# Performance work log

Hardware: AMD Instinct MI355X
Metric: run time of the kernel (lower is better)

The kernel has to match this reference:

```python
import jax, jax.numpy as jnp
import numpy as np

B, W = 32, 8            # batch, context window (2*winsize)
NCH, NCO = 4, 8         # padded chars / compos per target word
N_WORD, N_CHAR, N_COMPO, DIM = 32000, 8000, 1000, 300
N_NEG = int(N_WORD ** 0.75)  # 2392, per original: int(n_word ** neg_sample)
PAD = 1                 # idx == 1 is masked out in build_embedding
EPS = 1e-32


def setup_inputs() -> dict:
    key = jax.random.key(0)
    ks = jax.random.split(key, 7)
    return {
        "word_emb": jax.random.normal(ks[0], (N_WORD, DIM), jnp.float32) * 0.01,
        "char_emb": jax.random.normal(ks[1], (N_CHAR, DIM), jnp.float32) * 0.01,
        "compo_emb": jax.random.normal(ks[2], (N_COMPO, DIM), jnp.float32) * 0.01,
        "chars": jax.random.randint(ks[3], (B, NCH), 0, N_CHAR),
        "compos": jax.random.randint(ks[4], (B, NCO), 0, N_COMPO),
        "ctx_words": jax.random.randint(ks[5], (B, W), 0, N_WORD),
        "noise": jax.random.randint(ks[6], (B, W, N_NEG), 0, N_WORD),
    }


def _bag(emb, idx):
    # masked embedding-bag: sum emb[idx] over last idx axis where idx != PAD
    vecs = emb[idx]  # [..., L, DIM]
    mask = (idx != PAD)[..., None].astype(emb.dtype)
    return (vecs * mask).sum(-2)


def reference(word_emb, char_emb, compo_emb, chars, compos, ctx_words, noise):
    # prediction vector = char-bag + compo-bag   -> [B, DIM]
    tgt = _bag(char_emb, chars) + _bag(compo_emb, compos)
    # context word vectors (single idx, masked)  -> [B, W, DIM]
    ctx = _bag(word_emb, ctx_words[:, :, None])
    # positive term: sum log sigmoid(tgt . ctx)
    s_pos = jnp.einsum("bd,bwd->bw", tgt, ctx)
    log_target = jnp.log(jax.nn.sigmoid(s_pos)).sum()
    # negative-sampling term over noise word embeddings [B, W, N_NEG, DIM]
    noise_vec = word_emb[noise]
    s_neg = jnp.einsum("bd,bwnd->bwn", tgt, noise_vec)
    sum_log_noise = jnp.log(jax.nn.sigmoid(-s_neg) + EPS).sum()
    loss = log_target + sum_log_noise
    return -loss / B
```

## Files before the change

### kernel.cpp

```cpp
#include <hip/hip_runtime.h>

#define N_WORD 32000
#define DIM    300
#define KP     320
#define LROW   328
#define BQ     32
#define WW     8
#define NNEG   2392
#define PERB   (WW*NNEG)
#define NTOT   (BQ*PERB)
#define VB     64
#define NGEMB  (N_WORD/VB)
#define NBLK3  1024

typedef __attribute__((ext_vector_type(8))) short short8;
typedef __attribute__((ext_vector_type(4))) float f32x4;

__device__ __forceinline__ unsigned f2b2(float lo, float hi) {
  unsigned ul = __builtin_bit_cast(unsigned, lo);
  unsigned uh = __builtin_bit_cast(unsigned, hi);
  ul = (ul + 0x7FFF + ((ul >> 16) & 1)) >> 16;
  uh = (uh + 0x7FFF + ((uh >> 16) & 1));
  return (ul & 0xFFFFu) | (uh & 0xFFFF0000u);
}
__device__ __forceinline__ unsigned short f2b(float f) {
  unsigned u = __builtin_bit_cast(unsigned, f);
  return (unsigned short)((u + 0x7FFF + ((u >> 16) & 1)) >> 16);
}

__global__ __launch_bounds__(256) void prep_kernel(
    const float* __restrict__ char_emb, const float* __restrict__ compo_emb,
    const int* __restrict__ chars, const int* __restrict__ compos,
    unsigned short* __restrict__ tgt_bf) {
  int b = blockIdx.x;
  for (int d = threadIdx.x; d < KP; d += 256) {
    float a = 0.f;
    if (d < DIM) {
      #pragma unroll
      for (int j = 0; j < 4; ++j) {
        int c = chars[b*4 + j];
        if (c != 1) a += char_emb[(size_t)c*DIM + d];
      }
      #pragma unroll
      for (int j = 0; j < 8; ++j) {
        int c = compos[b*8 + j];
        if (c != 1) a += compo_emb[(size_t)c*DIM + d];
      }
    }
    tgt_bf[b*KP + d] = (d < DIM) ? f2b(a) : (unsigned short)0;
  }
}

__global__ __launch_bounds__(256) void s_gemm_kernel(
    const float4* __restrict__ w4, const unsigned* __restrict__ tgtbf2,
    float* __restrict__ S) {
  __shared__ unsigned short wt[VB][LROW];
  __shared__ unsigned short tt[BQ][LROW];
  int tid = threadIdx.x, wv = tid >> 6, lane = tid & 63;
  int vbase = blockIdx.x * VB;

  for (int idx = tid; idx < VB*75; idx += 256) {
    float4 x = w4[(size_t)vbase*75 + idx];
    int row = idx / 75, col = idx - row*75;
    unsigned* dst = (unsigned*)&wt[row][col*4];
    dst[0] = f2b2(x.x, x.y);
    dst[1] = f2b2(x.z, x.w);
  }
  if (tid < VB) {
    unsigned* dst = (unsigned*)&wt[tid][300];
    #pragma unroll
    for (int j = 0; j < 10; ++j) dst[j] = 0;
  }
  for (int idx = tid; idx < BQ*(KP/2); idx += 256) {
    int row = idx / (KP/2), kk = idx - row*(KP/2);
    ((unsigned*)&tt[row][0])[kk] = tgtbf2[idx];
  }
  __syncthreads();

  int ln = lane & 15, g = lane >> 4;
  const unsigned short* brow  = &wt[wv*16 + ln][g*8];
  const unsigned short* arow0 = &tt[ln][g*8];
  const unsigned short* arow1 = &tt[16 + ln][g*8];
  f32x4 acc0 = {0.f,0.f,0.f,0.f}, acc1 = {0.f,0.f,0.f,0.f};
  #pragma unroll
  for (int kb = 0; kb < KP/32; ++kb) {
    short8 bf = *(const short8*)(brow  + kb*32);
    short8 a0 = *(const short8*)(arow0 + kb*32);
    short8 a1 = *(const short8*)(arow1 + kb*32);
    acc0 = __builtin_amdgcn_mfma_f32_16x16x32_bf16(a0, bf, acc0, 0, 0, 0);
    acc1 = __builtin_amdgcn_mfma_f32_16x16x32_bf16(a1, bf, acc1, 0, 0, 0);
  }

  int v = vbase + wv*16 + ln;
  #pragma unroll
  for (int r = 0; r < 4; ++r) {
    int b0 = g*4 + r;
    S[(size_t)b0*N_WORD + v]        = acc0[r];
    S[(size_t)(b0 + 16)*N_WORD + v] = acc1[r];
  }
}

__global__ __launch_bounds__(256) void loss_kernel(
    const float* __restrict__ S, const int* __restrict__ noise,
    const int* __restrict__ ctx, float* __restrict__ partials) {
  float a = 0.f;
  for (int i = blockIdx.x*256 + threadIdx.x; i < NTOT; i += 256*NBLK3) {
    int b = i / PERB;
    int idx = noise[i];
    float s = S[(size_t)b*N_WORD + idx];
    a += __logf(1.f/(1.f + __expf(s)) + 1e-32f);
  }
  if (blockIdx.x == 0) {
    int i = threadIdx.x;
    int c = ctx[i];
    float s = (c == 1) ? 0.f : S[(size_t)(i >> 3)*N_WORD + c];
    a += __logf(1.f/(1.f + __expf(-s)));
  }
  #pragma unroll
  for (int off = 32; off > 0; off >>= 1) a += __shfl_down(a, off);
  __shared__ float wsum[4];
  int lane = threadIdx.x & 63, wid = threadIdx.x >> 6;
  if (lane == 0) wsum[wid] = a;
  __syncthreads();
  if (threadIdx.x == 0)
    partials[blockIdx.x] = wsum[0] + wsum[1] + wsum[2] + wsum[3];
}

__global__ __launch_bounds__(256) void final_kernel(
    const float* __restrict__ partials, float* __restrict__ out) {
  double a = 0.0;
  for (int i = threadIdx.x; i < NBLK3; i += 256) a += (double)partials[i];
  #pragma unroll
  for (int off = 32; off > 0; off >>= 1) a += __shfl_down(a, off);
  __shared__ double w2[4];
  int lane = threadIdx.x & 63, wid = threadIdx.x >> 6;
  if (lane == 0) w2[wid] = a;
  __syncthreads();
  if (threadIdx.x == 0)
    out[0] = (float)(-(w2[0] + w2[1] + w2[2] + w2[3]) / (double)BQ);
}

extern "C" void kernel_launch(void* const* d_in, const int* in_sizes, int n_in,
                              void* d_out, int out_size, void* d_ws, size_t ws_size,
                              hipStream_t stream) {
  const float* word_emb  = (const float*)d_in[0];
  const float* char_emb  = (const float*)d_in[1];
  const float* compo_emb = (const float*)d_in[2];
  const int*   chars     = (const int*)d_in[3];
  const int*   compos    = (const int*)d_in[4];
  const int*   ctx       = (const int*)d_in[5];
  const int*   noise     = (const int*)d_in[6];
  float* out = (float*)d_out;

  char* ws = (char*)d_ws;
  unsigned short* tgt_bf   = (unsigned short*)(ws);
  float*          S        = (float*)(ws + 20480);
  float*          partials = (float*)(ws + 20480 + 4096000);

  prep_kernel<<<BQ, 256, 0, stream>>>(char_emb, compo_emb, chars, compos, tgt_bf);
  s_gemm_kernel<<<NGEMB, 256, 0, stream>>>(
      (const float4*)word_emb, (const unsigned*)tgt_bf, S);
  loss_kernel<<<NBLK3, 256, 0, stream>>>(S, noise, ctx, partials);
  final_kernel<<<1, 256, 0, stream>>>(partials, out);
}
```

Before: 32.99 us.

## Drop LDS staging in S GEMM and fuse final reduction via fixed-point atomics

The GEMM kernel now reads word embedding rows straight from global memory into MFMA operands and converts them to bf16 in registers, with no shared-memory staging or barrier. It also reads target vectors directly from global memory and raises occupancy through launch bounds. The separate final reduction kernel is removed: each loss block adds a fixed-point encoded partial with a 64-bit atomic, and the last block to finish writes the output. This saves one launch and the LDS round trip, at the cost of less coalesced global loads and some fixed-point quantization of the partial sums.

New measurement: 58.40 us. 77.0% more time.

```diff
diff --git a/kernel.cpp b/kernel.cpp
--- a/kernel.cpp
+++ b/kernel.cpp
@@ -3,15 +3,13 @@
 #define N_WORD 32000
 #define DIM    300
 #define KP     320
-#define LROW   328
 #define BQ     32
 #define WW     8
 #define NNEG   2392
 #define PERB   (WW*NNEG)
 #define NTOT   (BQ*PERB)
-#define VB     64
-#define NGEMB  (N_WORD/VB)
 #define NBLK3  1024
+#define FSCALE 268435456.0
 
 typedef __attribute__((ext_vector_type(8))) short short8;
 typedef __attribute__((ext_vector_type(4))) float f32x4;
@@ -31,7 +29,9 @@
 __global__ __launch_bounds__(256) void prep_kernel(
     const float* __restrict__ char_emb, const float* __restrict__ compo_emb,
     const int* __restrict__ chars, const int* __restrict__ compos,
-    unsigned short* __restrict__ tgt_bf) {
+    unsigned short* __restrict__ tgt_bf,
+    unsigned long long* __restrict__ acc, int* __restrict__ cnt) {
+  if (blockIdx.x == 0 && threadIdx.x == 0) { *acc = 0ULL; *cnt = 0; }
   int b = blockIdx.x;
   for (int d = threadIdx.x; d < KP; d += 256) {
     float a = 0.f;
@@ -51,47 +51,46 @@
   }
 }
 
-__global__ __launch_bounds__(256) void s_gemm_kernel(
-    const float4* __restrict__ w4, const unsigned* __restrict__ tgtbf2,
+__global__ __launch_bounds__(256, 2) void s_gemm_kernel(
+    const float* __restrict__ w, const unsigned short* __restrict__ tgt_bf,
     float* __restrict__ S) {
-  __shared__ unsigned short wt[VB][LROW];
-  __shared__ unsigned short tt[BQ][LROW];
   int tid = threadIdx.x, wv = tid >> 6, lane = tid & 63;
-  int vbase = blockIdx.x * VB;
+  int ln = lane & 15, g = lane >> 4;
+  int v = blockIdx.x*64 + wv*16 + ln;
+  const float* rp = w + (size_t)v*DIM;
+  const unsigned short* ar0 = tgt_bf + ln*KP;
+  const unsigned short* ar1 = tgt_bf + (16 + ln)*KP;
 
-  for (int idx = tid; idx < VB*75; idx += 256) {
-    float4 x = w4[(size_t)vbase*75 + idx];
-    int row = idx / 75, col = idx - row*75;
-    unsigned* dst = (unsigned*)&wt[row][col*4];
-    dst[0] = f2b2(x.x, x.y);
-    dst[1] = f2b2(x.z, x.w);
-  }
-  if (tid < VB) {
-    unsigned* dst = (unsigned*)&wt[tid][300];
-    #pragma unroll
-    for (int j = 0; j < 10; ++j) dst[j] = 0;
-  }
-  for (int idx = tid; idx < BQ*(KP/2); idx += 256) {
-    int row = idx / (KP/2), kk = idx - row*(KP/2);
-    ((unsigned*)&tt[row][0])[kk] = tgtbf2[idx];
-  }
-  __syncthreads();
-
-  int ln = lane & 15, g = lane >> 4;
-  const unsigned short* brow  = &wt[wv*16 + ln][g*8];
-  const unsigned short* arow0 = &tt[ln][g*8];
-  const unsigned short* arow1 = &tt[16 + ln][g*8];
   f32x4 acc0 = {0.f,0.f,0.f,0.f}, acc1 = {0.f,0.f,0.f,0.f};
   #pragma unroll
-  for (int kb = 0; kb < KP/32; ++kb) {
-    short8 bf = *(const short8*)(brow  + kb*32);
-    short8 a0 = *(const short8*)(arow0 + kb*32);
-    short8 a1 = *(const short8*)(arow1 + kb*32);
+  for (int kb = 0; kb < 9; ++kb) {
+    const float* p = rp + kb*32 + g*8;
+    float4 f0 = *(const float4*)p;
+    float4 f1 = *(const float4*)(p + 4);
+    short8 bf;
+    unsigned* bu = (unsigned*)&bf;
+    bu[0] = f2b2(f0.x, f0.y); bu[1] = f2b2(f0.z, f0.w);
+    bu[2] = f2b2(f1.x, f1.y); bu[3] = f2b2(f1.z, f1.w);
+    short8 a0 = *(const short8*)(ar0 + kb*32 + g*8);
+    short8 a1 = *(const short8*)(ar1 + kb*32 + g*8);
+    acc0 = __builtin_amdgcn_mfma_f32_16x16x32_bf16(a0, bf, acc0, 0, 0, 0);
+    acc1 = __builtin_amdgcn_mfma_f32_16x16x32_bf16(a1, bf, acc1, 0, 0, 0);
+  }
+  {
+    int k0 = 288 + g*8;
+    float4 f0 = {0.f,0.f,0.f,0.f}, f1 = {0.f,0.f,0.f,0.f};
+    if (k0 < 300)     f0 = *(const float4*)(rp + k0);
+    if (k0 + 4 < 300) f1 = *(const float4*)(rp + k0 + 4);
+    short8 bf;
+    unsigned* bu = (unsigned*)&bf;
+    bu[0] = f2b2(f0.x, f0.y); bu[1] = f2b2(f0.z, f0.w);
+    bu[2] = f2b2(f1.x, f1.y); bu[3] = f2b2(f1.z, f1.w);
+    short8 a0 = *(const short8*)(ar0 + 288 + g*8);
+    short8 a1 = *(const short8*)(ar1 + 288 + g*8);
     acc0 = __builtin_amdgcn_mfma_f32_16x16x32_bf16(a0, bf, acc0, 0, 0, 0);
     acc1 = __builtin_amdgcn_mfma_f32_16x16x32_bf16(a1, bf, acc1, 0, 0, 0);
   }
 
-  int v = vbase + wv*16 + ln;
   #pragma unroll
   for (int r = 0; r < 4; ++r) {
     int b0 = g*4 + r;
@@ -102,7 +101,8 @@
 
 __global__ __launch_bounds__(256) void loss_kernel(
     const float* __restrict__ S, const int* __restrict__ noise,
-    const int* __restrict__ ctx, float* __restrict__ partials) {
+    const int* __restrict__ ctx, unsigned long long* __restrict__ acc,
+    int* __restrict__ cnt, float* __restrict__ out) {
   float a = 0.f;
   for (int i = blockIdx.x*256 + threadIdx.x; i < NTOT; i += 256*NBLK3) {
     int b = i / PERB;
@@ -122,22 +122,18 @@
   int lane = threadIdx.x & 63, wid = threadIdx.x >> 6;
   if (lane == 0) wsum[wid] = a;
   __syncthreads();
-  if (threadIdx.x == 0)
-    partials[blockIdx.x] = wsum[0] + wsum[1] + wsum[2] + wsum[3];
-}
-
-__global__ __launch_bounds__(256) void final_kernel(
-    const float* __restrict__ partials, float* __restrict__ out) {
-  double a = 0.0;
-  for (int i = threadIdx.x; i < NBLK3; i += 256) a += (double)partials[i];
-  #pragma unroll
-  for (int off = 32; off > 0; off >>= 1) a += __shfl_down(a, off);
-  __shared__ double w2[4];
-  int lane = threadIdx.x & 63, wid = threadIdx.x >> 6;
-  if (lane == 0) w2[wid] = a;
-  __syncthreads();
-  if (threadIdx.x == 0)
-    out[0] = (float)(-(w2[0] + w2[1] + w2[2] + w2[3]) / (double)BQ);
+  if (threadIdx.x == 0) {
+    float partial = wsum[0] + wsum[1] + wsum[2] + wsum[3];
+    unsigned long long enc =
+        (unsigned long long)(long long)llrintf(partial * (float)FSCALE);
+    atomicAdd(acc, enc);
+    __threadfence();
+    int old = atomicAdd(cnt, 1);
+    if (old == NBLK3 - 1) {
+      long long tot = (long long)atomicAdd(acc, 0ULL);
+      out[0] = (float)(-((double)tot / FSCALE) / (double)BQ);
+    }
+  }
 }
 
 extern "C" void kernel_launch(void* const* d_in, const int* in_sizes, int n_in,
@@ -153,13 +149,13 @@
   float* out = (float*)d_out;
 
   char* ws = (char*)d_ws;
-  unsigned short* tgt_bf   = (unsigned short*)(ws);
-  float*          S        = (float*)(ws + 20480);
-  float*          partials = (float*)(ws + 20480 + 4096000);
+  unsigned short*     tgt_bf = (unsigned short*)(ws);
+  float*              S      = (float*)(ws + 20480);
+  unsigned long long* acc    = (unsigned long long*)(ws + 20480 + 4096000);
+  int*                cnt    = (int*)(ws + 20480 + 4096000 + 8);
 
-  prep_kernel<<<BQ, 256, 0, stream>>>(char_emb, compo_emb, chars, compos, tgt_bf);
-  s_gemm_kernel<<<NGEMB, 256, 0, stream>>>(
-      (const float4*)word_emb, (const unsigned*)tgt_bf, S);
-  loss_kernel<<<NBLK3, 256, 0, stream>>>(S, noise, ctx, partials);
-  final_kernel<<<1, 256, 0, stream>>>(partials, out);
+  prep_kernel<<<BQ, 256, 0, stream>>>(char_emb, compo_emb, chars, compos,
+                                      tgt_bf, acc, cnt);
+  s_gemm_kernel<<<N_WORD/64, 256, 0, stream>>>(word_emb, tgt_bf, S);
+  loss_kernel<<<NBLK3, 256, 0, stream>>>(S, noise, ctx, acc, cnt, out);
 }
```
